# Kernel tuning notes

Measured on AMD Instinct MI355X. Metric: run time of the kernel, lower is better.

## Reference

```python
import jax, jax.numpy as jnp
import numpy as np

SIZES = [384, 160, 128, 96, 1]   # aev_length followed by hidden sizes (ANI-1 config)
N_SPECIES = 4                    # H, C, N, O
N_LAYERS = 4
CELU_ALPHA = 0.1
B, A = 128, 512                  # molecules, atoms per molecule


def setup_inputs() -> dict:
    key = jax.random.key(0)
    ks = jax.random.split(key, 2 + 2 * N_LAYERS)
    inp = {
        "fullaev": jax.random.normal(ks[0], (B, A, SIZES[0]), dtype=jnp.float32),
        "species": jax.random.randint(ks[1], (A,), 0, N_SPECIES, dtype=jnp.int32),
    }
    # Per-species stacked Linear params, torch default init: U(-1/sqrt(fan_in), 1/sqrt(fan_in))
    for l in range(N_LAYERS):
        bound = 1.0 / np.sqrt(SIZES[l])
        inp[f"W{l}"] = jax.random.uniform(ks[2 + 2 * l], (N_SPECIES, SIZES[l + 1], SIZES[l]),
                                          dtype=jnp.float32, minval=-bound, maxval=bound)
        inp[f"b{l}"] = jax.random.uniform(ks[3 + 2 * l], (N_SPECIES, SIZES[l + 1]),
                                          dtype=jnp.float32, minval=-bound, maxval=bound)
    return inp


def reference(fullaev, species, W0, b0, W1, b1, W2, b2, W3, b3):
    # fullaev: [B, A, aev_len]; species: [A] int route ids.
    # Equivalent to the per-atom Python loop: each atom goes through its
    # species' MLP; gather the per-atom weight matrices and do one batched GEMM per layer.
    Ws = (W0, W1, W2, W3)
    bs = (b0, b1, b2, b3)
    y = fullaev
    for l in range(N_LAYERS):
        Wa = Ws[l][species]          # [A, out, in] gathered per atom
        ba = bs[l][species]          # [A, out]
        y = jnp.einsum('bai,aoi->bao', y, Wa) + ba[None, :, :]
        if l < N_LAYERS - 1:
            y = jax.nn.celu(y, alpha=CELU_ALPHA)
    # stack over atoms + sum reducer over atom dim, then squeeze -> [B]
    return jnp.squeeze(jnp.sum(y, axis=1), axis=-1)
```

## Files before the change

### kernel.cpp

```cpp
#include <hip/hip_runtime.h>
#include <hip/hip_bf16.h>


typedef float f32x4 __attribute__((ext_vector_type(4)));
typedef short s16x8 __attribute__((ext_vector_type(8)));

#define NMOL   128
#define NATOM  512
#define AEV    384
#define Y0LD   168
#define Y1LD   136
#define Y2LD   104

#define PL0    61440
#define PL1    20480
#define PL2    12288
#define BASE0  0
#define BASE1  245760
#define BASE2  327680
#define WP_BYTE_OFF 262144

__device__ __forceinline__ ushort f2bf(float f) {
    uint u = __float_as_uint(f);
    return (ushort)((u + 0x7fffu + ((u >> 16) & 1u)) >> 16);
}
__device__ __forceinline__ float bf2f(ushort h) {
    return __uint_as_float(((uint)h) << 16);
}
__device__ __forceinline__ float celu_f(float v) {
    return fmaxf(v, 0.0f) + fminf(0.1f * (__expf(10.0f * v) - 1.0f), 0.0f);
}
__device__ __forceinline__ uint pk2bf(float x, float y) {
    __hip_bfloat162 h2;
    h2.x = __float2bfloat16(x);
    h2.y = __float2bfloat16(y);
    return *(uint*)&h2;
}

__global__ __launch_bounds__(256) void prep_kernel(
    const float* __restrict__ W0, const float* __restrict__ W1,
    const float* __restrict__ W2, ushort* __restrict__ Wp)
{
    const int idx = blockIdx.x * 256 + threadIdx.x;
    int n, k0, KS;
    size_t base;
    const float* src;
    if (idx < 30720) {
        const int s = idx / 7680, r = idx % 7680;
        n = r / 48; k0 = (r % 48) * 8; KS = 12;
        src = W0 + (size_t)idx * 8;
        base = BASE0 + (size_t)s * PL0;
    } else if (idx < 40960) {
        const int i2 = idx - 30720;
        const int s = i2 / 2560, r = i2 % 2560;
        n = r / 20; k0 = (r % 20) * 8; KS = 5;
        src = W1 + (size_t)i2 * 8;
        base = BASE1 + (size_t)s * PL1;
    } else {
        const int i2 = idx - 40960;
        const int s = i2 / 1536, r = i2 % 1536;
        n = r / 16; k0 = (r % 16) * 8; KS = 4;
        src = W2 + (size_t)i2 * 8;
        base = BASE2 + (size_t)s * PL2;
    }
    const float4 v0 = *(const float4*)(src);
    const float4 v1 = *(const float4*)(src + 4);
    const size_t fo = (size_t)((((n >> 4) * KS + (k0 >> 5)) * 64
                                + ((k0 & 31) >> 3) * 16 + (n & 15)) * 8);
    uint4 w;
    w.x = (uint)f2bf(v0.x) | ((uint)f2bf(v0.y) << 16);
    w.y = (uint)f2bf(v0.z) | ((uint)f2bf(v0.w) << 16);
    w.z = (uint)f2bf(v1.x) | ((uint)f2bf(v1.y) << 16);
    w.w = (uint)f2bf(v1.z) | ((uint)f2bf(v1.w) << 16);
    *(uint4*)(Wp + base + fo) = w;
}

__global__ __attribute__((amdgpu_flat_work_group_size(512, 512),
                          amdgpu_waves_per_eu(4, 4)))
void ani_mfma_kernel(
    const float* __restrict__ aev, const int* __restrict__ species,
    const ushort* __restrict__ Wp,
    const float* __restrict__ b0, const float* __restrict__ b1,
    const float* __restrict__ b2,
    const float* __restrict__ W3, const float* __restrict__ b3,
    float* __restrict__ partial)
{
    __shared__ __align__(16) ushort y0buf[NMOL * Y0LD];
    __shared__ __align__(16) ushort y1buf[NMOL * Y1LD];

    const int a    = blockIdx.x;
    const int tid  = threadIdx.x;
    const int lane = tid & 63;
    const int wid  = tid >> 6;

    const int s = species[a];
    const ushort* Bh0 = Wp + BASE0 + (size_t)s * PL0;
    const ushort* Bh1 = Wp + BASE1 + (size_t)s * PL1;
    const ushort* Bh2 = Wp + BASE2 + (size_t)s * PL2;
    const float* b0s = b0 + s * 160;
    const float* b1s = b1 + s * 128;
    const float* b2s = b2 + s * 96;
    const float* w3s = W3 + s * 96;
    const float  bb3 = b3[s];

    const f32x4 zero = {0.f, 0.f, 0.f, 0.f};

    {
        const int mgrp0 = wid >> 1;
        const int ngrp0 = wid & 1;
        const float* arow = aev + ((size_t)(mgrp0 * 32 + (lane & 15)) * NATOM + a) * AEV
                            + (lane >> 4) * 8;
        const size_t AMF = (size_t)16 * NATOM * AEV;

        f32x4 acc0[2][5];
        #pragma unroll
        for (int mf = 0; mf < 2; ++mf)
            #pragma unroll
            for (int nf = 0; nf < 5; ++nf) acc0[mf][nf] = zero;

        #pragma unroll
        for (int gks = 0; gks < 12; ++gks) {
            s16x8 ah[2];
            #pragma unroll
            for (int mf = 0; mf < 2; ++mf) {
                const float* ap = arow + mf * AMF + gks * 32;
                const float4 lo = *(const float4*)(ap);
                const float4 hi = *(const float4*)(ap + 4);
                union { s16x8 v; uint u[4]; } r;
                r.u[0] = pk2bf(lo.x, lo.y);
                r.u[1] = pk2bf(lo.z, lo.w);
                r.u[2] = pk2bf(hi.x, hi.y);
                r.u[3] = pk2bf(hi.z, hi.w);
                ah[mf] = r.v;
            }
            #pragma unroll
            for (int nf = 0; nf < 5; ++nf) {
                const s16x8 bh = *(const s16x8*)(
                    Bh0 + ((size_t)((ngrp0 * 5 + nf) * 12 + gks) * 64 + lane) * 8);
                acc0[0][nf] = __builtin_amdgcn_mfma_f32_16x16x32_bf16(ah[0], bh, acc0[0][nf], 0, 0, 0);
                acc0[1][nf] = __builtin_amdgcn_mfma_f32_16x16x32_bf16(ah[1], bh, acc0[1][nf], 0, 0, 0);
            }
        }

        #pragma unroll
        for (int nf = 0; nf < 5; ++nf) {
            const int n = (ngrp0 * 5 + nf) * 16 + (lane & 15);
            const float bv = b0s[n];
            #pragma unroll
            for (int mf = 0; mf < 2; ++mf) {
                #pragma unroll
                for (int r = 0; r < 4; ++r) {
                    const int row = mgrp0 * 32 + mf * 16 + (lane >> 4) * 4 + r;
                    y0buf[row * Y0LD + n] = f2bf(celu_f(acc0[mf][nf][r] + bv));
                }
            }
        }
    }

    const int mgrp = wid >> 2;
    const int ngrp = wid & 3;
    const bool has3 = (ngrp < 2);
    s16x8 b1r[2][5];
    #pragma unroll
    for (int ks = 0; ks < 5; ++ks) {
        b1r[0][ks] = *(const s16x8*)(Bh1 + ((size_t)((ngrp    ) * 5 + ks) * 64 + lane) * 8);
        b1r[1][ks] = *(const s16x8*)(Bh1 + ((size_t)((ngrp + 4) * 5 + ks) * 64 + lane) * 8);
    }
    __syncthreads();

    f32x4 acc1[4][2];
    #pragma unroll
    for (int mf = 0; mf < 4; ++mf) { acc1[mf][0] = zero; acc1[mf][1] = zero; }
    #pragma unroll
    for (int ks = 0; ks < 5; ++ks) {
        s16x8 ah[4];
        #pragma unroll
        for (int mf = 0; mf < 4; ++mf)
            ah[mf] = *(const s16x8*)(y0buf + (mgrp * 64 + mf * 16 + (lane & 15)) * Y0LD
                                     + ks * 32 + (lane >> 4) * 8);
        #pragma unroll
        for (int mf = 0; mf < 4; ++mf) {
            acc1[mf][0] = __builtin_amdgcn_mfma_f32_16x16x32_bf16(ah[mf], b1r[0][ks], acc1[mf][0], 0, 0, 0);
            acc1[mf][1] = __builtin_amdgcn_mfma_f32_16x16x32_bf16(ah[mf], b1r[1][ks], acc1[mf][1], 0, 0, 0);
        }
    }

    s16x8 b2r[2][4];
    #pragma unroll
    for (int ks = 0; ks < 4; ++ks)
        b2r[0][ks] = *(const s16x8*)(Bh2 + ((size_t)((ngrp) * 4 + ks) * 64 + lane) * 8);
    if (has3) {
        #pragma unroll
        for (int ks = 0; ks < 4; ++ks)
            b2r[1][ks] = *(const s16x8*)(Bh2 + ((size_t)((ngrp + 4) * 4 + ks) * 64 + lane) * 8);
    }

    #pragma unroll
    for (int t = 0; t < 2; ++t) {
        const int n = (ngrp + 4 * t) * 16 + (lane & 15);
        const float bv = b1s[n];
        #pragma unroll
        for (int mf = 0; mf < 4; ++mf) {
            #pragma unroll
            for (int r = 0; r < 4; ++r) {
                const int row = mgrp * 64 + mf * 16 + (lane >> 4) * 4 + r;
                y1buf[row * Y1LD + n] = f2bf(celu_f(acc1[mf][t][r] + bv));
            }
        }
    }
    __syncthreads();

    f32x4 acc2[4][2];
    #pragma unroll
    for (int mf = 0; mf < 4; ++mf) { acc2[mf][0] = zero; acc2[mf][1] = zero; }
    #pragma unroll
    for (int ks = 0; ks < 4; ++ks) {
        s16x8 ah[4];
        #pragma unroll
        for (int mf = 0; mf < 4; ++mf)
            ah[mf] = *(const s16x8*)(y1buf + (mgrp * 64 + mf * 16 + (lane & 15)) * Y1LD
                                     + ks * 32 + (lane >> 4) * 8);
        #pragma unroll
        for (int mf = 0; mf < 4; ++mf) {
            acc2[mf][0] = __builtin_amdgcn_mfma_f32_16x16x32_bf16(ah[mf], b2r[0][ks], acc2[mf][0], 0, 0, 0);
            if (has3)
                acc2[mf][1] = __builtin_amdgcn_mfma_f32_16x16x32_bf16(ah[mf], b2r[1][ks], acc2[mf][1], 0, 0, 0);
        }
    }
    __syncthreads();

    #pragma unroll
    for (int t = 0; t < 2; ++t) {
        if (t == 0 || has3) {
            const int n = (ngrp + 4 * t) * 16 + (lane & 15);
            const float bv = b2s[n];
            #pragma unroll
            for (int mf = 0; mf < 4; ++mf) {
                #pragma unroll
                for (int r = 0; r < 4; ++r) {
                    const int row = mgrp * 64 + mf * 16 + (lane >> 4) * 4 + r;
                    y0buf[row * Y2LD + n] = f2bf(celu_f(acc2[mf][t][r] + bv));
                }
            }
        }
    }
    __syncthreads();

    {
        float* red = (float*)y1buf;
        const int m = tid & (NMOL - 1);
        const int q = tid >> 7;
        float accv = 0.f;
        #pragma unroll
        for (int ii = 0; ii < 24; ++ii) {
            const int i = q * 24 + ii;
            accv = fmaf(w3s[i], bf2f(y0buf[m * Y2LD + i]), accv);
        }
        red[q * NMOL + m] = accv;
        __syncthreads();
        if (tid < NMOL) {
            const float sm = red[tid] + red[NMOL + tid] + red[2 * NMOL + tid]
                           + red[3 * NMOL + tid] + bb3;
            partial[(size_t)a * NMOL + tid] = sm;
        }
    }
}

__global__ __launch_bounds__(256) void reduce_kernel(
    const float* __restrict__ partial, float* __restrict__ out)
{
    __shared__ float red[256];
    const int m = blockIdx.x;
    const int t = threadIdx.x;
    float sv = partial[(size_t)t * NMOL + m] + partial[(size_t)(t + 256) * NMOL + m];
    red[t] = sv;
    __syncthreads();
    #pragma unroll
    for (int w = 128; w > 0; w >>= 1) {
        if (t < w) red[t] += red[t + w];
        __syncthreads();
    }
    if (t == 0) out[m] = red[0];
}

extern "C" void kernel_launch(void* const* d_in, const int* in_sizes, int n_in,
                              void* d_out, int out_size, void* d_ws, size_t ws_size,
                              hipStream_t stream) {
    const float* aev     = (const float*)d_in[0];
    const int*   species = (const int*)  d_in[1];
    const float* W0 = (const float*)d_in[2];
    const float* b0 = (const float*)d_in[3];
    const float* W1 = (const float*)d_in[4];
    const float* b1 = (const float*)d_in[5];
    const float* W2 = (const float*)d_in[6];
    const float* b2 = (const float*)d_in[7];
    const float* W3 = (const float*)d_in[8];
    const float* b3 = (const float*)d_in[9];
    float* out     = (float*)d_out;
    float* partial = (float*)d_ws;
    ushort* Wp     = (ushort*)((char*)d_ws + WP_BYTE_OFF);

    prep_kernel<<<184, 256, 0, stream>>>(W0, W1, W2, Wp);
    ani_mfma_kernel<<<NATOM, 512, 0, stream>>>(aev, species, Wp,
                                               b0, b1, b2, W3, b3, partial);
    reduce_kernel<<<NMOL, 256, 0, stream>>>(partial, out);
}
```

Measured before the change: 52.22 us.

## Split molecules across two blocks and stream AEV via async global-to-LDS loads

Each atom is now processed by two blocks of 64 molecules each, which halves shared-memory use per block and raises the waves-per-EU target from 4 to 8 for more occupancy. The layer-0 AEV tiles are fetched with global_load_lds into double-buffered, XOR-swizzled LDS instead of direct strided global loads into registers, overlapping the next tile's load with the current MFMAs. Layer-0 work is redistributed so the waves cover the N dimension with a conditional third fragment. The cost is a barrier per K-step and layer-0 weight fragments being read twice per atom, once by each half-block.

```diff
diff --git a/kernel.cpp b/kernel.cpp
--- a/kernel.cpp
+++ b/kernel.cpp
@@ -8,6 +8,7 @@
 #define NMOL   128
 #define NATOM  512
 #define AEV    384
+#define MT     64
 #define Y0LD   168
 #define Y1LD   136
 #define Y2LD   104
@@ -19,6 +20,9 @@
 #define BASE1  245760
 #define BASE2  327680
 #define WP_BYTE_OFF 262144
+
+typedef const __attribute__((address_space(1))) void* gas_ptr;
+typedef __attribute__((address_space(3))) void* las_ptr;
 
 __device__ __forceinline__ ushort f2bf(float f) {
     uint u = __float_as_uint(f);
@@ -76,7 +80,7 @@
 }
 
 __global__ __attribute__((amdgpu_flat_work_group_size(512, 512),
-                          amdgpu_waves_per_eu(4, 4)))
+                          amdgpu_waves_per_eu(8, 8)))
 void ani_mfma_kernel(
     const float* __restrict__ aev, const int* __restrict__ species,
     const ushort* __restrict__ Wp,
@@ -85,13 +89,18 @@
     const float* __restrict__ W3, const float* __restrict__ b3,
     float* __restrict__ partial)
 {
-    __shared__ __align__(16) ushort y0buf[NMOL * Y0LD];
-    __shared__ __align__(16) ushort y1buf[NMOL * Y1LD];
-
-    const int a    = blockIdx.x;
+    __shared__ __align__(16) unsigned char smemA[17408];
+    __shared__ __align__(16) unsigned char smemB[21504];
+
+    const int bid  = blockIdx.x;
+    const int a    = bid >> 1;
+    const int half = bid & 1;
     const int tid  = threadIdx.x;
     const int lane = tid & 63;
     const int wid  = tid >> 6;
+    const int mgrp = wid >> 2;
+    const int ngrp = wid & 3;
+    const bool has3 = (ngrp < 2);
 
     const int s = species[a];
     const ushort* Bh0 = Wp + BASE0 + (size_t)s * PL0;
@@ -103,83 +112,101 @@
     const float* w3s = W3 + s * 96;
     const float  bb3 = b3[s];
 
+    ushort* y0buf = (ushort*)smemB;
+    ushort* y1buf = (ushort*)smemA;
+
+    const int mol8 = lane >> 3;
+    const int swz  = (lane & 7) ^ mol8;
+    const char* gsrc = (const char*)(aev
+        + ((size_t)(half * MT + wid * 8 + mol8) * NATOM + a) * AEV) + swz * 16;
+    const int ldsbase = wid * 1024;
+
     const f32x4 zero = {0.f, 0.f, 0.f, 0.f};
+    f32x4 acc[2][3];
+    #pragma unroll
+    for (int mf = 0; mf < 2; ++mf)
+        #pragma unroll
+        for (int ti = 0; ti < 3; ++ti) acc[mf][ti] = zero;
 
     {
-        const int mgrp0 = wid >> 1;
-        const int ngrp0 = wid & 1;
-        const float* arow = aev + ((size_t)(mgrp0 * 32 + (lane & 15)) * NATOM + a) * AEV
-                            + (lane >> 4) * 8;
-        const size_t AMF = (size_t)16 * NATOM * AEV;
-
-        f32x4 acc0[2][5];
-        #pragma unroll
-        for (int mf = 0; mf < 2; ++mf)
-            #pragma unroll
-            for (int nf = 0; nf < 5; ++nf) acc0[mf][nf] = zero;
-
-        #pragma unroll
-        for (int gks = 0; gks < 12; ++gks) {
+        const int r0 = mgrp * 32 + (lane & 15);
+        const int c  = lane >> 4;
+
+        __builtin_amdgcn_global_load_lds((gas_ptr)(gsrc),
+                                         (las_ptr)(smemA + ldsbase), 16, 0, 0);
+        __syncthreads();
+
+        #pragma unroll
+        for (int t = 0; t < 12; ++t) {
+            if (t < 11)
+                __builtin_amdgcn_global_load_lds(
+                    (gas_ptr)(gsrc + (t + 1) * 128),
+                    (las_ptr)(smemA + (((t + 1) & 1) * 8192) + ldsbase), 16, 0, 0);
+
+            const float* Xb = (const float*)(smemA + (t & 1) * 8192);
             s16x8 ah[2];
             #pragma unroll
             for (int mf = 0; mf < 2; ++mf) {
-                const float* ap = arow + mf * AMF + gks * 32;
-                const float4 lo = *(const float4*)(ap);
-                const float4 hi = *(const float4*)(ap + 4);
-                union { s16x8 v; uint u[4]; } r;
-                r.u[0] = pk2bf(lo.x, lo.y);
-                r.u[1] = pk2bf(lo.z, lo.w);
-                r.u[2] = pk2bf(hi.x, hi.y);
-                r.u[3] = pk2bf(hi.z, hi.w);
-                ah[mf] = r.v;
-            }
-            #pragma unroll
-            for (int nf = 0; nf < 5; ++nf) {
-                const s16x8 bh = *(const s16x8*)(
-                    Bh0 + ((size_t)((ngrp0 * 5 + nf) * 12 + gks) * 64 + lane) * 8);
-                acc0[0][nf] = __builtin_amdgcn_mfma_f32_16x16x32_bf16(ah[0], bh, acc0[0][nf], 0, 0, 0);
-                acc0[1][nf] = __builtin_amdgcn_mfma_f32_16x16x32_bf16(ah[1], bh, acc0[1][nf], 0, 0, 0);
-            }
-        }
-
-        #pragma unroll
-        for (int nf = 0; nf < 5; ++nf) {
-            const int n = (ngrp0 * 5 + nf) * 16 + (lane & 15);
+                const int r = r0 + mf * 16;
+                const float* rowp = Xb + r * 32;
+                const f32x4 c0 = *(const f32x4*)(rowp + (((2 * c    ) ^ (r & 7)) * 4));
+                const f32x4 c1 = *(const f32x4*)(rowp + (((2 * c + 1) ^ (r & 7)) * 4));
+                union { s16x8 v; uint u[4]; } rr;
+                rr.u[0] = pk2bf(c0.x, c0.y);
+                rr.u[1] = pk2bf(c0.z, c0.w);
+                rr.u[2] = pk2bf(c1.x, c1.y);
+                rr.u[3] = pk2bf(c1.z, c1.w);
+                ah[mf] = rr.v;
+            }
+            #pragma unroll
+            for (int ti = 0; ti < 3; ++ti) {
+                if (ti < 2 || has3) {
+                    const s16x8 bh = *(const s16x8*)(
+                        Bh0 + ((size_t)((ngrp + 4 * ti) * 12 + t) * 64 + lane) * 8);
+                    acc[0][ti] = __builtin_amdgcn_mfma_f32_16x16x32_bf16(ah[0], bh, acc[0][ti], 0, 0, 0);
+                    acc[1][ti] = __builtin_amdgcn_mfma_f32_16x16x32_bf16(ah[1], bh, acc[1][ti], 0, 0, 0);
+                }
+            }
+            if (t < 11) __syncthreads();
+        }
+    }
+
+    s16x8 b1r[2][5];
+    #pragma unroll
+    for (int ks = 0; ks < 5; ++ks) {
+        b1r[0][ks] = *(const s16x8*)(Bh1 + ((size_t)((ngrp    ) * 5 + ks) * 64 + lane) * 8);
+        b1r[1][ks] = *(const s16x8*)(Bh1 + ((size_t)((ngrp + 4) * 5 + ks) * 64 + lane) * 8);
+    }
+
+    #pragma unroll
+    for (int ti = 0; ti < 3; ++ti) {
+        if (ti < 2 || has3) {
+            const int n = (ngrp + 4 * ti) * 16 + (lane & 15);
             const float bv = b0s[n];
             #pragma unroll
             for (int mf = 0; mf < 2; ++mf) {
                 #pragma unroll
                 for (int r = 0; r < 4; ++r) {
-                    const int row = mgrp0 * 32 + mf * 16 + (lane >> 4) * 4 + r;
-                    y0buf[row * Y0LD + n] = f2bf(celu_f(acc0[mf][nf][r] + bv));
+                    const int row = mgrp * 32 + mf * 16 + (lane >> 4) * 4 + r;
+                    y0buf[row * Y0LD + n] = f2bf(celu_f(acc[mf][ti][r] + bv));
                 }
             }
         }
     }
-
-    const int mgrp = wid >> 2;
-    const int ngrp = wid & 3;
-    const bool has3 = (ngrp < 2);
-    s16x8 b1r[2][5];
+    __syncthreads();
+
+    f32x4 acc1[2][2];
+    #pragma unroll
+    for (int mf = 0; mf < 2; ++mf) { acc1[mf][0] = zero; acc1[mf][1] = zero; }
     #pragma unroll
     for (int ks = 0; ks < 5; ++ks) {
-        b1r[0][ks] = *(const s16x8*)(Bh1 + ((size_t)((ngrp    ) * 5 + ks) * 64 + lane) * 8);
-        b1r[1][ks] = *(const s16x8*)(Bh1 + ((size_t)((ngrp + 4) * 5 + ks) * 64 + lane) * 8);
-    }
-    __syncthreads();
-
-    f32x4 acc1[4][2];
-    #pragma unroll
-    for (int mf = 0; mf < 4; ++mf) { acc1[mf][0] = zero; acc1[mf][1] = zero; }
-    #pragma unroll
-    for (int ks = 0; ks < 5; ++ks) {
-        s16x8 ah[4];
-        #pragma unroll
-        for (int mf = 0; mf < 4; ++mf)
-            ah[mf] = *(const s16x8*)(y0buf + (mgrp * 64 + mf * 16 + (lane & 15)) * Y0LD
+        s16x8 ah[2];
+        #pragma unroll
+        for (int mf = 0; mf < 2; ++mf)
+            ah[mf] = *(const s16x8*)(y0buf + (mgrp * 32 + mf * 16 + (lane & 15)) * Y0LD
                                      + ks * 32 + (lane >> 4) * 8);
         #pragma unroll
-        for (int mf = 0; mf < 4; ++mf) {
+        for (int mf = 0; mf < 2; ++mf) {
             acc1[mf][0] = __builtin_amdgcn_mfma_f32_16x16x32_bf16(ah[mf], b1r[0][ks], acc1[mf][0], 0, 0, 0);
             acc1[mf][1] = __builtin_amdgcn_mfma_f32_16x16x32_bf16(ah[mf], b1r[1][ks], acc1[mf][1], 0, 0, 0);
         }
@@ -200,28 +227,28 @@
         const int n = (ngrp + 4 * t) * 16 + (lane & 15);
         const float bv = b1s[n];
         #pragma unroll
-        for (int mf = 0; mf < 4; ++mf) {
+        for (int mf = 0; mf < 2; ++mf) {
             #pragma unroll
             for (int r = 0; r < 4; ++r) {
-                const int row = mgrp * 64 + mf * 16 + (lane >> 4) * 4 + r;
+                const int row = mgrp * 32 + mf * 16 + (lane >> 4) * 4 + r;
                 y1buf[row * Y1LD + n] = f2bf(celu_f(acc1[mf][t][r] + bv));
             }
         }
     }
     __syncthreads();
 
-    f32x4 acc2[4][2];
-    #pragma unroll
-    for (int mf = 0; mf < 4; ++mf) { acc2[mf][0] = zero; acc2[mf][1] = zero; }
+    f32x4 acc2[2][2];
+    #pragma unroll
+    for (int mf = 0; mf < 2; ++mf) { acc2[mf][0] = zero; acc2[mf][1] = zero; }
     #pragma unroll
     for (int ks = 0; ks < 4; ++ks) {
-        s16x8 ah[4];
-        #pragma unroll
-        for (int mf = 0; mf < 4; ++mf)
-            ah[mf] = *(const s16x8*)(y1buf + (mgrp * 64 + mf * 16 + (lane & 15)) * Y1LD
+        s16x8 ah[2];
+        #pragma unroll
+        for (int mf = 0; mf < 2; ++mf)
+            ah[mf] = *(const s16x8*)(y1buf + (mgrp * 32 + mf * 16 + (lane & 15)) * Y1LD
                                      + ks * 32 + (lane >> 4) * 8);
         #pragma unroll
-        for (int mf = 0; mf < 4; ++mf) {
+        for (int mf = 0; mf < 2; ++mf) {
             acc2[mf][0] = __builtin_amdgcn_mfma_f32_16x16x32_bf16(ah[mf], b2r[0][ks], acc2[mf][0], 0, 0, 0);
             if (has3)
                 acc2[mf][1] = __builtin_amdgcn_mfma_f32_16x16x32_bf16(ah[mf], b2r[1][ks], acc2[mf][1], 0, 0, 0);
@@ -235,10 +262,10 @@
             const int n = (ngrp + 4 * t) * 16 + (lane & 15);
             const float bv = b2s[n];
             #pragma unroll
-            for (int mf = 0; mf < 4; ++mf) {
+            for (int mf = 0; mf < 2; ++mf) {
                 #pragma unroll
                 for (int r = 0; r < 4; ++r) {
-                    const int row = mgrp * 64 + mf * 16 + (lane >> 4) * 4 + r;
+                    const int row = mgrp * 32 + mf * 16 + (lane >> 4) * 4 + r;
                     y0buf[row * Y2LD + n] = f2bf(celu_f(acc2[mf][t][r] + bv));
                 }
             }
@@ -247,21 +274,22 @@
     __syncthreads();
 
     {
-        float* red = (float*)y1buf;
-        const int m = tid & (NMOL - 1);
-        const int q = tid >> 7;
+        float* red = (float*)smemA;
+        const int m = tid & (MT - 1);
+        const int q = tid >> 6;
         float accv = 0.f;
         #pragma unroll
-        for (int ii = 0; ii < 24; ++ii) {
-            const int i = q * 24 + ii;
+        for (int ii = 0; ii < 12; ++ii) {
+            const int i = q * 12 + ii;
             accv = fmaf(w3s[i], bf2f(y0buf[m * Y2LD + i]), accv);
         }
-        red[q * NMOL + m] = accv;
+        red[q * MT + m] = accv;
         __syncthreads();
-        if (tid < NMOL) {
-            const float sm = red[tid] + red[NMOL + tid] + red[2 * NMOL + tid]
-                           + red[3 * NMOL + tid] + bb3;
-            partial[(size_t)a * NMOL + tid] = sm;
+        if (tid < MT) {
+            float sm = bb3;
+            #pragma unroll
+            for (int qq = 0; qq < 8; ++qq) sm += red[qq * MT + tid];
+            partial[(size_t)a * NMOL + half * MT + tid] = sm;
         }
     }
 }
@@ -301,7 +329,7 @@
     ushort* Wp     = (ushort*)((char*)d_ws + WP_BYTE_OFF);
 
     prep_kernel<<<184, 256, 0, stream>>>(W0, W1, W2, Wp);
-    ani_mfma_kernel<<<NATOM, 512, 0, stream>>>(aev, species, Wp,
-                                               b0, b1, b2, W3, b3, partial);
+    ani_mfma_kernel<<<NATOM * 2, 512, 0, stream>>>(aev, species, Wp,
+                                                   b0, b1, b2, W3, b3, partial);
     reduce_kernel<<<NMOL, 256, 0, stream>>>(partial, out);
 }
```

Result: faster. 42.95 us (-17.8%).

## Give each wave a private 16-molecule slice across all layers, dropping block barriers

Applied to the files above, without the earlier changes.

Each wave now owns 16 molecules and runs the whole MLP chain for them alone. It uses wave-private LDS buffers, and the fp32 AEV input is staged into LDS as bf16 through a double buffer. This removes every __syncthreads, and the final reduction becomes a lane shuffle instead of a block-level shared-memory reduce. In exchange, every wave must fetch all weight fragments for every layer with no register reuse across M fragments, which multiplies weight loads from cache. The weight-packing helper also switches to pk2bf.

```diff
diff --git a/kernel.cpp b/kernel.cpp
--- a/kernel.cpp
+++ b/kernel.cpp
@@ -8,6 +8,11 @@
 #define NMOL   128
 #define NATOM  512
 #define AEV    384
+
+#define XLD    36
+#define XBUF   576
+#define ASL    2176
+#define BSL    2688
 #define Y0LD   168
 #define Y1LD   136
 #define Y2LD   104
@@ -68,10 +73,10 @@
     const size_t fo = (size_t)((((n >> 4) * KS + (k0 >> 5)) * 64
                                 + ((k0 & 31) >> 3) * 16 + (n & 15)) * 8);
     uint4 w;
-    w.x = (uint)f2bf(v0.x) | ((uint)f2bf(v0.y) << 16);
-    w.y = (uint)f2bf(v0.z) | ((uint)f2bf(v0.w) << 16);
-    w.z = (uint)f2bf(v1.x) | ((uint)f2bf(v1.y) << 16);
-    w.w = (uint)f2bf(v1.z) | ((uint)f2bf(v1.w) << 16);
+    w.x = pk2bf(v0.x, v0.y);
+    w.y = pk2bf(v0.z, v0.w);
+    w.z = pk2bf(v1.x, v1.y);
+    w.w = pk2bf(v1.z, v1.w);
     *(uint4*)(Wp + base + fo) = w;
 }
 
@@ -85,13 +90,14 @@
     const float* __restrict__ W3, const float* __restrict__ b3,
     float* __restrict__ partial)
 {
-    __shared__ __align__(16) ushort y0buf[NMOL * Y0LD];
-    __shared__ __align__(16) ushort y1buf[NMOL * Y1LD];
+    __shared__ __align__(16) ushort smemA[8 * ASL];
+    __shared__ __align__(16) ushort smemB[8 * BSL];
 
     const int a    = blockIdx.x;
     const int tid  = threadIdx.x;
     const int lane = tid & 63;
     const int wid  = tid >> 6;
+    const int mol0 = wid * 16;
 
     const int s = species[a];
     const ushort* Bh0 = Wp + BASE0 + (size_t)s * PL0;
@@ -103,166 +109,125 @@
     const float* w3s = W3 + s * 96;
     const float  bb3 = b3[s];
 
+    ushort* Xw  = smemA + wid * ASL;
+    ushort* Y1w = smemA + wid * ASL;
+    ushort* Y0w = smemB + wid * BSL;
+    ushort* Y2w = smemB + wid * BSL;
+
     const f32x4 zero = {0.f, 0.f, 0.f, 0.f};
 
-    {
-        const int mgrp0 = wid >> 1;
-        const int ngrp0 = wid & 1;
-        const float* arow = aev + ((size_t)(mgrp0 * 32 + (lane & 15)) * NATOM + a) * AEV
-                            + (lane >> 4) * 8;
-        const size_t AMF = (size_t)16 * NATOM * AEV;
-
-        f32x4 acc0[2][5];
-        #pragma unroll
-        for (int mf = 0; mf < 2; ++mf)
+    const int srow = lane >> 2;
+    const int sc   = lane & 3;
+    const float* sp = aev + ((size_t)(mol0 + srow) * NATOM + a) * AEV + sc * 8;
+
+    auto stage = [&](int t, int b) {
+        const float4 v0 = *(const float4*)(sp + t * 32);
+        const float4 v1 = *(const float4*)(sp + t * 32 + 4);
+        uint4 w;
+        w.x = pk2bf(v0.x, v0.y);
+        w.y = pk2bf(v0.z, v0.w);
+        w.z = pk2bf(v1.x, v1.y);
+        w.w = pk2bf(v1.z, v1.w);
+        *(uint4*)(Xw + b * XBUF + srow * XLD + sc * 8) = w;
+    };
+
+    f32x4 acc0[10];
+    #pragma unroll
+    for (int nf = 0; nf < 10; ++nf) acc0[nf] = zero;
+
+    stage(0, 0);
+    {
+        const ushort* arow = Xw + (lane & 15) * XLD + (lane >> 4) * 8;
+        #pragma unroll
+        for (int gks = 0; gks < 12; ++gks) {
+            if (gks < 11) stage(gks + 1, (gks + 1) & 1);
+            const s16x8 ah = *(const s16x8*)(arow + (gks & 1) * XBUF);
             #pragma unroll
-            for (int nf = 0; nf < 5; ++nf) acc0[mf][nf] = zero;
-
-        #pragma unroll
-        for (int gks = 0; gks < 12; ++gks) {
-            s16x8 ah[2];
+            for (int nf = 0; nf < 10; ++nf) {
+                const s16x8 bh = *(const s16x8*)(
+                    Bh0 + ((size_t)(nf * 12 + gks) * 64 + lane) * 8);
+                acc0[nf] = __builtin_amdgcn_mfma_f32_16x16x32_bf16(ah, bh, acc0[nf], 0, 0, 0);
+            }
+        }
+    }
+    #pragma unroll
+    for (int nf = 0; nf < 10; ++nf) {
+        const int n = nf * 16 + (lane & 15);
+        const float bv = b0s[n];
+        #pragma unroll
+        for (int r = 0; r < 4; ++r) {
+            const int row = (lane >> 4) * 4 + r;
+            Y0w[row * Y0LD + n] = f2bf(celu_f(acc0[nf][r] + bv));
+        }
+    }
+
+    f32x4 acc1[8];
+    #pragma unroll
+    for (int nf = 0; nf < 8; ++nf) acc1[nf] = zero;
+    {
+        const ushort* arow = Y0w + (lane & 15) * Y0LD + (lane >> 4) * 8;
+        #pragma unroll
+        for (int ks = 0; ks < 5; ++ks) {
+            const s16x8 ah = *(const s16x8*)(arow + ks * 32);
             #pragma unroll
-            for (int mf = 0; mf < 2; ++mf) {
-                const float* ap = arow + mf * AMF + gks * 32;
-                const float4 lo = *(const float4*)(ap);
-                const float4 hi = *(const float4*)(ap + 4);
-                union { s16x8 v; uint u[4]; } r;
-                r.u[0] = pk2bf(lo.x, lo.y);
-                r.u[1] = pk2bf(lo.z, lo.w);
-                r.u[2] = pk2bf(hi.x, hi.y);
-                r.u[3] = pk2bf(hi.z, hi.w);
-                ah[mf] = r.v;
+            for (int nf = 0; nf < 8; ++nf) {
+                const s16x8 bh = *(const s16x8*)(
+                    Bh1 + ((size_t)(nf * 5 + ks) * 64 + lane) * 8);
+                acc1[nf] = __builtin_amdgcn_mfma_f32_16x16x32_bf16(ah, bh, acc1[nf], 0, 0, 0);
             }
+        }
+    }
+    #pragma unroll
+    for (int nf = 0; nf < 8; ++nf) {
+        const int n = nf * 16 + (lane & 15);
+        const float bv = b1s[n];
+        #pragma unroll
+        for (int r = 0; r < 4; ++r) {
+            const int row = (lane >> 4) * 4 + r;
+            Y1w[row * Y1LD + n] = f2bf(celu_f(acc1[nf][r] + bv));
+        }
+    }
+
+    f32x4 acc2[6];
+    #pragma unroll
+    for (int nf = 0; nf < 6; ++nf) acc2[nf] = zero;
+    {
+        const ushort* arow = Y1w + (lane & 15) * Y1LD + (lane >> 4) * 8;
+        #pragma unroll
+        for (int ks = 0; ks < 4; ++ks) {
+            const s16x8 ah = *(const s16x8*)(arow + ks * 32);
             #pragma unroll
-            for (int nf = 0; nf < 5; ++nf) {
+            for (int nf = 0; nf < 6; ++nf) {
                 const s16x8 bh = *(const s16x8*)(
-                    Bh0 + ((size_t)((ngrp0 * 5 + nf) * 12 + gks) * 64 + lane) * 8);
-                acc0[0][nf] = __builtin_amdgcn_mfma_f32_16x16x32_bf16(ah[0], bh, acc0[0][nf], 0, 0, 0);
-                acc0[1][nf] = __builtin_amdgcn_mfma_f32_16x16x32_bf16(ah[1], bh, acc0[1][nf], 0, 0, 0);
+                    Bh2 + ((size_t)(nf * 4 + ks) * 64 + lane) * 8);
+                acc2[nf] = __builtin_amdgcn_mfma_f32_16x16x32_bf16(ah, bh, acc2[nf], 0, 0, 0);
             }
         }
-
-        #pragma unroll
-        for (int nf = 0; nf < 5; ++nf) {
-            const int n = (ngrp0 * 5 + nf) * 16 + (lane & 15);
-            const float bv = b0s[n];
-            #pragma unroll
-            for (int mf = 0; mf < 2; ++mf) {
-                #pragma unroll
-                for (int r = 0; r < 4; ++r) {
-                    const int row = mgrp0 * 32 + mf * 16 + (lane >> 4) * 4 + r;
-                    y0buf[row * Y0LD + n] = f2bf(celu_f(acc0[mf][nf][r] + bv));
-                }
-            }
-        }
-    }
-
-    const int mgrp = wid >> 2;
-    const int ngrp = wid & 3;
-    const bool has3 = (ngrp < 2);
-    s16x8 b1r[2][5];
-    #pragma unroll
-    for (int ks = 0; ks < 5; ++ks) {
-        b1r[0][ks] = *(const s16x8*)(Bh1 + ((size_t)((ngrp    ) * 5 + ks) * 64 + lane) * 8);
-        b1r[1][ks] = *(const s16x8*)(Bh1 + ((size_t)((ngrp + 4) * 5 + ks) * 64 + lane) * 8);
-    }
-    __syncthreads();
-
-    f32x4 acc1[4][2];
-    #pragma unroll
-    for (int mf = 0; mf < 4; ++mf) { acc1[mf][0] = zero; acc1[mf][1] = zero; }
-    #pragma unroll
-    for (int ks = 0; ks < 5; ++ks) {
-        s16x8 ah[4];
-        #pragma unroll
-        for (int mf = 0; mf < 4; ++mf)
-            ah[mf] = *(const s16x8*)(y0buf + (mgrp * 64 + mf * 16 + (lane & 15)) * Y0LD
-                                     + ks * 32 + (lane >> 4) * 8);
-        #pragma unroll
-        for (int mf = 0; mf < 4; ++mf) {
-            acc1[mf][0] = __builtin_amdgcn_mfma_f32_16x16x32_bf16(ah[mf], b1r[0][ks], acc1[mf][0], 0, 0, 0);
-            acc1[mf][1] = __builtin_amdgcn_mfma_f32_16x16x32_bf16(ah[mf], b1r[1][ks], acc1[mf][1], 0, 0, 0);
-        }
-    }
-
-    s16x8 b2r[2][4];
-    #pragma unroll
-    for (int ks = 0; ks < 4; ++ks)
-        b2r[0][ks] = *(const s16x8*)(Bh2 + ((size_t)((ngrp) * 4 + ks) * 64 + lane) * 8);
-    if (has3) {
-        #pragma unroll
-        for (int ks = 0; ks < 4; ++ks)
-            b2r[1][ks] = *(const s16x8*)(Bh2 + ((size_t)((ngrp + 4) * 4 + ks) * 64 + lane) * 8);
-    }
-
-    #pragma unroll
-    for (int t = 0; t < 2; ++t) {
-        const int n = (ngrp + 4 * t) * 16 + (lane & 15);
-        const float bv = b1s[n];
-        #pragma unroll
-        for (int mf = 0; mf < 4; ++mf) {
-            #pragma unroll
-            for (int r = 0; r < 4; ++r) {
-                const int row = mgrp * 64 + mf * 16 + (lane >> 4) * 4 + r;
-                y1buf[row * Y1LD + n] = f2bf(celu_f(acc1[mf][t][r] + bv));
-            }
-        }
-    }
-    __syncthreads();
-
-    f32x4 acc2[4][2];
-    #pragma unroll
-    for (int mf = 0; mf < 4; ++mf) { acc2[mf][0] = zero; acc2[mf][1] = zero; }
-    #pragma unroll
-    for (int ks = 0; ks < 4; ++ks) {
-        s16x8 ah[4];
-        #pragma unroll
-        for (int mf = 0; mf < 4; ++mf)
-            ah[mf] = *(const s16x8*)(y1buf + (mgrp * 64 + mf * 16 + (lane & 15)) * Y1LD
-                                     + ks * 32 + (lane >> 4) * 8);
-        #pragma unroll
-        for (int mf = 0; mf < 4; ++mf) {
-            acc2[mf][0] = __builtin_amdgcn_mfma_f32_16x16x32_bf16(ah[mf], b2r[0][ks], acc2[mf][0], 0, 0, 0);
-            if (has3)
-                acc2[mf][1] = __builtin_amdgcn_mfma_f32_16x16x32_bf16(ah[mf], b2r[1][ks], acc2[mf][1], 0, 0, 0);
-        }
-    }
-    __syncthreads();
-
-    #pragma unroll
-    for (int t = 0; t < 2; ++t) {
-        if (t == 0 || has3) {
-            const int n = (ngrp + 4 * t) * 16 + (lane & 15);
-            const float bv = b2s[n];
-            #pragma unroll
-            for (int mf = 0; mf < 4; ++mf) {
-                #pragma unroll
-                for (int r = 0; r < 4; ++r) {
-                    const int row = mgrp * 64 + mf * 16 + (lane >> 4) * 4 + r;
-                    y0buf[row * Y2LD + n] = f2bf(celu_f(acc2[mf][t][r] + bv));
-                }
-            }
-        }
-    }
-    __syncthreads();
-
-    {
-        float* red = (float*)y1buf;
-        const int m = tid & (NMOL - 1);
-        const int q = tid >> 7;
+    }
+    #pragma unroll
+    for (int nf = 0; nf < 6; ++nf) {
+        const int n = nf * 16 + (lane & 15);
+        const float bv = b2s[n];
+        #pragma unroll
+        for (int r = 0; r < 4; ++r) {
+            const int row = (lane >> 4) * 4 + r;
+            Y2w[row * Y2LD + n] = f2bf(celu_f(acc2[nf][r] + bv));
+        }
+    }
+
+    {
+        const int row = lane >> 2;
+        const int q   = lane & 3;
         float accv = 0.f;
         #pragma unroll
         for (int ii = 0; ii < 24; ++ii) {
             const int i = q * 24 + ii;
-            accv = fmaf(w3s[i], bf2f(y0buf[m * Y2LD + i]), accv);
-        }
-        red[q * NMOL + m] = accv;
-        __syncthreads();
-        if (tid < NMOL) {
-            const float sm = red[tid] + red[NMOL + tid] + red[2 * NMOL + tid]
-                           + red[3 * NMOL + tid] + bb3;
-            partial[(size_t)a * NMOL + tid] = sm;
-        }
+            accv = fmaf(w3s[i], bf2f(Y2w[row * Y2LD + i]), accv);
+        }
+        accv += __shfl_xor(accv, 1);
+        accv += __shfl_xor(accv, 2);
+        if (q == 0)
+            partial[(size_t)a * NMOL + mol0 + row] = accv + bb3;
     }
 }
 
```

Result: slower. 67.82 us (median of 2 runs) (+29.9%).
